# Kernel optimization log

Hardware: AMD Instinct MI355X
Metric: run time of the kernel (lower is better)

## Reference

```python
import jax, jax.numpy as jnp
import numpy as np

D = 300   # hidden dim (Linear(300,300))
L = 160   # seq len, forced by W3 = Linear(160,1)


def _linear(x, W, b):
    # torch Linear: x @ W.T + b, W is (out, in)
    return jnp.matmul(x, W.T) + b


def setup_inputs() -> dict:
    key = jax.random.key(0)
    ks = jax.random.split(key, 16)
    B = 1024
    s = 1.0 / np.sqrt(D)
    inp = {
        'T_feature': jax.random.normal(ks[0], (B, L, D), jnp.float32),
        'CD_feature': jax.random.normal(ks[1], (B, L, D), jnp.float32),
        'Wproj': jax.random.normal(ks[2], (D, D), jnp.float32) * s,
        'bproj': jnp.zeros((D,), jnp.float32),
        'WqT_w': jax.random.normal(ks[3], (D, D), jnp.float32) * s,
        'WqT_b': jnp.zeros((D,), jnp.float32),
        'WqCD_w': jax.random.normal(ks[4], (D, D), jnp.float32) * s,
        'WqCD_b': jnp.zeros((D,), jnp.float32),
        'WkT_w': jax.random.normal(ks[5], (D, D), jnp.float32) * s,
        'WkT_b': jnp.zeros((D,), jnp.float32),
        'WkCD_w': jax.random.normal(ks[6], (D, D), jnp.float32) * s,
        'WkCD_b': jnp.zeros((D,), jnp.float32),
        'W3_w': jax.random.normal(ks[7], (1, L), jnp.float32) * (1.0 / np.sqrt(L)),
        'W3_b': jnp.zeros((1,), jnp.float32),
    }
    return inp


def reference(T_feature, CD_feature, Wproj, bproj, WqT_w, WqT_b, WqCD_w, WqCD_b,
              WkT_w, WkT_b, WkCD_w, WkCD_b, W3_w, W3_b):
    sqrt_d = jnp.sqrt(jnp.float32(D))
    proj_T = _linear(T_feature, Wproj, bproj)     # (B, L, D)
    proj_CD = _linear(CD_feature, Wproj, bproj)   # (B, L, D)

    # N_tensor @ proj_T is just the mean over tokens (weights 1/Len)
    mean_T = jnp.mean(proj_T, axis=1, keepdims=True)          # (B, 1, D)
    qT = _linear(mean_T, WqT_w, WqT_b)                        # (B, 1, D)
    kT = _linear(proj_T, WkT_w, WkT_b)                        # (B, L, D)
    alphaT = jnp.einsum('bqd,bkd->bqk', qT, kT) / sqrt_d      # (B, 1, L)
    ZT = jax.nn.sigmoid(alphaT)

    qCD = _linear(proj_CD, WqCD_w, WqCD_b)                    # (B, L, D)
    kCD = _linear(proj_CD, WkCD_w, WkCD_b)                    # (B, L, D)
    alphaCD = jnp.einsum('bqd,bkd->bqk', qCD, kCD) / sqrt_d   # (B, L, L)
    ZCD = jax.nn.sigmoid(alphaCD)

    # The per-token loop+cat is a plain broadcast multiply: Mt[:,i,:] = ZCD[:,i,:] * ZT[:,0,:]
    Mt = ZCD * ZT                                             # (B, L, L)
    alpha_f = jax.nn.softmax(_linear(Mt, W3_w, W3_b), axis=1) # (B, L, 1)

    # Second loop is a per-token scalar scale: HCD[:,i,:] = alpha_f[:,i,0] * proj_CD[:,i,:]
    HCD = alpha_f * proj_CD                                   # (B, L, D)
    return (proj_T, HCD)
```

## Files before the change

kernel.cpp:

```cpp
#include <hip/hip_runtime.h>
#include <hip/hip_bf16.h>


typedef __attribute__((ext_vector_type(8))) short short8;
typedef __attribute__((ext_vector_type(4))) float f32x4;

#define DP 320

__device__ __forceinline__ unsigned short f2bf(float x) {
  unsigned int u = __builtin_bit_cast(unsigned int, x);
  u += 0x7FFFu + ((u >> 16) & 1u);
  return (unsigned short)(u >> 16);
}
__device__ __forceinline__ float bf2f(unsigned short h) {
  unsigned int u = ((unsigned int)h) << 16;
  return __builtin_bit_cast(float, u);
}
__device__ __forceinline__ void gload16(const void* g, void* l) {
  __builtin_amdgcn_global_load_lds(
      (const __attribute__((address_space(1))) unsigned int*)g,
      (__attribute__((address_space(3))) unsigned int*)l, 16, 0, 0);
}
__device__ __forceinline__ float sigm(float x) { return 1.0f / (1.0f + __expf(-x)); }
__device__ __forceinline__ int swz640(int row, int g) { return row * 640 + ((g ^ (row & 7)) << 4); }
__device__ __forceinline__ int swzY(int row, int g) { return row * 128 + ((g ^ (row & 7)) << 4); }

__global__ void wb_k(const float* __restrict__ W, unsigned short* __restrict__ Wb) {
  int n = blockIdx.x, k = threadIdx.x;
  unsigned short v = 0;
  if (n < 300 && k < 300) v = f2bf(W[n * 300 + k]);
  Wb[n * DP + k] = v;
}

__global__ void crossdot_k(const float* __restrict__ Wa, const float* __restrict__ ba,
                           const float* __restrict__ Wc, const float* __restrict__ bc,
                           unsigned short* __restrict__ out_h, float* __restrict__ out_f,
                           float scale) {
  int n = blockIdx.x, c = threadIdx.x;
  float v = 0.f;
  if (n <= 300 && c <= 300) {
    for (int o = 0; o < 300; ++o) {
      float a = (c < 300) ? Wa[o * 300 + c] : ba[o];
      float b = (n < 300) ? Wc[o * 300 + n] : bc[o];
      v += a * b;
    }
    v *= scale;
  }
  if (out_h) out_h[n * DP + c] = f2bf(v);
  else       out_f[n * DP + c] = v;
}

__global__ __launch_bounds__(512)
void gemm_k(const float* __restrict__ Tsrc, const float* __restrict__ CDsrc,
            const unsigned short* __restrict__ Wb, const float* __restrict__ bias,
            float* __restrict__ Of, unsigned short* __restrict__ Oh) {
  __shared__ __align__(16) unsigned short As[2][128 * 40];
  __shared__ __align__(16) unsigned short Bs[2][320 * 40];
  const int tid = threadIdx.x, wid = tid >> 6, lane = tid & 63;
  const int mode = blockIdx.y;
  const float* __restrict__ A = mode ? CDsrc : Tsrc;
  const long m0 = (long)blockIdx.x * 128;
  const int lr = lane & 15, lk = (lane >> 4) * 8;
  const int rm = (wid >> 2) * 64, cn = (wid & 3) * 80;

  f32x4 acc[4][5];
#pragma unroll
  for (int i = 0; i < 4; ++i)
#pragma unroll
    for (int j = 0; j < 5; ++j) acc[i][j] = (f32x4){0.f, 0.f, 0.f, 0.f};

  auto stageA = [&](int buf, int k0) {
    const int row = tid >> 2, cg = (tid & 3) * 8;
    const float* p = A + (m0 + row) * 300 + k0 + cg;
    short8 h;
    if (k0 + cg + 8 <= 300) {
      f32x4 x0 = *(const f32x4*)p, x1 = *(const f32x4*)(p + 4);
#pragma unroll
      for (int j = 0; j < 4; ++j) { h[j] = (short)f2bf(x0[j]); h[j + 4] = (short)f2bf(x1[j]); }
    } else {
#pragma unroll
      for (int j = 0; j < 8; ++j) {
        float v = (k0 + cg + j < 300) ? p[j] : 0.f;
        h[j] = (short)f2bf(v);
      }
    }
    *(short8*)&As[buf][row * 40 + cg] = h;
  };
  auto stageB = [&](int buf, int k0) {
#pragma unroll
    for (int it = 0; it < 3; ++it) {
      int idx = tid + it * 512;
      if (idx < 1280) {
        int row = idx >> 2, cg = (idx & 3) * 8;
        short8 h = *(const short8*)(Wb + row * DP + k0 + cg);
        *(short8*)&Bs[buf][row * 40 + cg] = h;
      }
    }
  };

  stageA(0, 0); stageB(0, 0);
  __syncthreads();
  int buf = 0;
  for (int kc = 0; kc < 10; ++kc) {
    if (kc < 9) { stageA(buf ^ 1, (kc + 1) * 32); stageB(buf ^ 1, (kc + 1) * 32); }
    short8 a[4], bb[5];
#pragma unroll
    for (int mf = 0; mf < 4; ++mf)
      a[mf] = *(const short8*)&As[buf][(rm + mf * 16 + lr) * 40 + lk];
#pragma unroll
    for (int nf = 0; nf < 5; ++nf)
      bb[nf] = *(const short8*)&Bs[buf][(cn + nf * 16 + lr) * 40 + lk];
#pragma unroll
    for (int mf = 0; mf < 4; ++mf)
#pragma unroll
      for (int nf = 0; nf < 5; ++nf)
        acc[mf][nf] = __builtin_amdgcn_mfma_f32_16x16x32_bf16(a[mf], bb[nf], acc[mf][nf], 0, 0, 0);
    __syncthreads();
    buf ^= 1;
  }

#pragma unroll
  for (int mf = 0; mf < 4; ++mf)
#pragma unroll
    for (int nf = 0; nf < 5; ++nf) {
      const int col = cn + nf * 16 + lr;
      const float bv = (col < 300) ? bias[col] : 0.f;
#pragma unroll
      for (int r = 0; r < 4; ++r) {
        const long row = m0 + rm + mf * 16 + (lane >> 4) * 4 + r;
        float v = acc[mf][nf][r] + bv;
        if (mode == 0) {
          if (col < 300) Of[row * 300 + col] = v;
        } else {
          unsigned short u = (col < 300) ? f2bf(v)
                            : ((col == 300) ? f2bf(1.0f) : (unsigned short)0);
          Oh[row * DP + col] = u;
        }
      }
    }
}

__global__ __launch_bounds__(320)
void gate_k(const float* __restrict__ projT, const float* __restrict__ Pmat,
            float* __restrict__ ZT) {
  __shared__ float mt[304];
  __shared__ float vv[304];
  const int b = blockIdx.x, tid = threadIdx.x, wid = tid >> 6, lane = tid & 63;
  const float* p = projT + (size_t)b * 48000;
  if (tid < 300) {
    float s = 0.f;
#pragma unroll 4
    for (int l = 0; l < 160; ++l) s += p[l * 300 + tid];
    mt[tid] = s * (1.0f / 160.0f);
  }
  __syncthreads();
  if (tid <= 300) {
    float s = Pmat[300 * DP + tid];
    for (int a = 0; a < 300; ++a) s += Pmat[a * DP + tid] * mt[a];
    vv[tid] = s;
  }
  __syncthreads();
  for (int j = wid * 32; j < wid * 32 + 32; ++j) {
    const float* row = p + j * 300;
    float s = 0.f;
    for (int c = lane; c < 300; c += 64) s += vv[c] * row[c];
#pragma unroll
    for (int m = 1; m < 64; m <<= 1) s += __shfl_xor(s, m, 64);
    if (lane == 0) ZT[b * 160 + j] = sigm(s + vv[300]);
  }
}

__global__ __launch_bounds__(640)
void finale_k(const unsigned short* __restrict__ P, const unsigned short* __restrict__ Maug,
              const float* __restrict__ ZT, const float* __restrict__ W3w,
              float* __restrict__ out) {
  __shared__ __align__(16) unsigned short Ps[160 * 320];
  __shared__ __align__(16) unsigned short Ms[32 * 320];
  __shared__ __align__(16) unsigned short Ys[160 * 64];
  __shared__ float t_arr[160];
  __shared__ float s_part[5][160];
  __shared__ float s_arr[160];
  __shared__ float red0;

  const int b = blockIdx.x, tid = threadIdx.x, wid = tid >> 6, lane = tid & 63;
  const int lr = lane & 15, hi = lane >> 4;
  const unsigned short* Pb = P + (size_t)b * 160 * DP;

  if (tid < 160) t_arr[tid] = ZT[b * 160 + tid] * W3w[tid];

#pragma unroll
  for (int it = 0; it < 10; ++it) {
    int o = it * 640 + tid;
    int row = o / 40, g = o - row * 40;
    gload16(Pb + row * DP + ((g ^ (row & 7)) << 3),
            (char*)Ps + ((it * 640 + (wid << 6)) << 4));
  }
  short8 mreg[2];
  int mrow[2], mg[2];
#pragma unroll
  for (int it = 0; it < 2; ++it) {
    int idx = tid + it * 640;
    mrow[it] = idx / 40; mg[it] = idx - mrow[it] * 40;
    mreg[it] = *(const short8*)(Maug + mrow[it] * DP + mg[it] * 8);
  }
  __syncthreads();
#pragma unroll
  for (int it = 0; it < 2; ++it)
    *(short8*)((char*)Ms + swz640(mrow[it], mg[it])) = mreg[it];
  short8 a_pre[10];
#pragma unroll
  for (int kk = 0; kk < 10; ++kk)
    a_pre[kk] = *(const short8*)((const char*)Ps + swz640(16 * wid + lr, kk * 4 + hi));
  __syncthreads();

  f32x4 acc_s[5][2];
#pragma unroll
  for (int i = 0; i < 5; ++i)
#pragma unroll
    for (int j = 0; j < 2; ++j) acc_s[i][j] = (f32x4){0.f, 0.f, 0.f, 0.f};
  const int wm = wid / 5, wn = wid - wm * 5;

  for (int nc = 0; nc < 10; ++nc) {
    if (nc < 9) {
#pragma unroll
      for (int it = 0; it < 2; ++it)
        mreg[it] = *(const short8*)(Maug + ((nc + 1) * 32 + mrow[it]) * DP + mg[it] * 8);
    }
    f32x4 accy0 = (f32x4){0.f, 0.f, 0.f, 0.f}, accy1 = accy0;
#pragma unroll
    for (int kk = 0; kk < 10; ++kk) {
      short8 b0 = *(const short8*)((const char*)Ms + swz640(lr, kk * 4 + hi));
      short8 b1 = *(const short8*)((const char*)Ms + swz640(16 + lr, kk * 4 + hi));
      accy0 = __builtin_amdgcn_mfma_f32_16x16x32_bf16(a_pre[kk], b0, accy0, 0, 0, 0);
      accy1 = __builtin_amdgcn_mfma_f32_16x16x32_bf16(a_pre[kk], b1, accy1, 0, 0, 0);
    }
    __syncthreads();
#pragma unroll
    for (int r = 0; r < 4; ++r) {
      int row = 16 * wid + hi * 4 + r;
      int c0 = lr, c1 = 16 + lr;
      *(unsigned short*)((char*)Ys + swzY(row, c0 >> 3) + ((c0 & 7) << 1)) = f2bf(accy0[r]);
      *(unsigned short*)((char*)Ys + swzY(row, c1 >> 3) + ((c1 & 7) << 1)) = f2bf(accy1[r]);
    }
    if (nc < 9) {
#pragma unroll
      for (int it = 0; it < 2; ++it)
        *(short8*)((char*)Ms + swz640(mrow[it], mg[it])) = mreg[it];
    }
    __syncthreads();
#pragma unroll
    for (int mf = 0; mf < 5; ++mf) {
      short8 a = *(const short8*)((const char*)Ys + swzY(80 * wm + mf * 16 + lr, hi));
#pragma unroll
      for (int nf = 0; nf < 2; ++nf) {
        short8 bv = *(const short8*)((const char*)Ps + swz640(32 * wn + nf * 16 + lr, nc * 4 + hi));
        acc_s[mf][nf] = __builtin_amdgcn_mfma_f32_16x16x32_bf16(a, bv, acc_s[mf][nf], 0, 0, 0);
      }
    }
    __syncthreads();
  }

  float tv0 = t_arr[32 * wn + lr], tv1 = t_arr[32 * wn + 16 + lr];
  float pp[5][4];
#pragma unroll
  for (int mf = 0; mf < 5; ++mf)
#pragma unroll
    for (int r = 0; r < 4; ++r)
      pp[mf][r] = sigm(acc_s[mf][0][r]) * tv0 + sigm(acc_s[mf][1][r]) * tv1;
#pragma unroll
  for (int m = 1; m < 16; m <<= 1)
#pragma unroll
    for (int mf = 0; mf < 5; ++mf)
#pragma unroll
      for (int r = 0; r < 4; ++r)
        pp[mf][r] += __shfl_xor(pp[mf][r], m, 64);
  if (lr == 0) {
#pragma unroll
    for (int mf = 0; mf < 5; ++mf)
#pragma unroll
      for (int r = 0; r < 4; ++r)
        s_part[wn][80 * wm + mf * 16 + hi * 4 + r] = pp[mf][r];
  }
  __syncthreads();
  if (tid < 160)
    s_arr[tid] = s_part[0][tid] + s_part[1][tid] + s_part[2][tid] + s_part[3][tid] + s_part[4][tid];
  __syncthreads();
  if (wid == 0) {
    float v0 = s_arr[lane], v1 = s_arr[lane + 64];
    float v2 = (lane < 32) ? s_arr[lane + 128] : -3.0e38f;
    float mx = fmaxf(fmaxf(v0, v1), v2);
#pragma unroll
    for (int m = 1; m < 64; m <<= 1) mx = fmaxf(mx, __shfl_xor(mx, m, 64));
    float e0 = __expf(v0 - mx), e1 = __expf(v1 - mx);
    float e2 = (lane < 32) ? __expf(v2 - mx) : 0.f;
    s_arr[lane] = e0; s_arr[lane + 64] = e1;
    if (lane < 32) s_arr[lane + 128] = e2;
    float sm = e0 + e1 + e2;
#pragma unroll
    for (int m = 1; m < 64; m <<= 1) sm += __shfl_xor(sm, m, 64);
    if (lane == 0) red0 = 1.0f / sm;
  }
  __syncthreads();
  const float inv = red0;
  float* ob = out + (size_t)b * 48000;
  for (int e = tid; e < 48000; e += 640) {
    int i = e / 300, c = e - i * 300;
    unsigned short pv = *(const unsigned short*)((const char*)Ps + swz640(i, c >> 3) + ((c & 7) << 1));
    ob[e] = s_arr[i] * inv * bf2f(pv);
  }
}

extern "C" void kernel_launch(void* const* d_in, const int* in_sizes, int n_in,
                              void* d_out, int out_size, void* d_ws, size_t ws_size,
                              hipStream_t stream) {
  (void)in_sizes; (void)n_in; (void)out_size; (void)ws_size;
  const float* T      = (const float*)d_in[0];
  const float* CD     = (const float*)d_in[1];
  const float* Wproj  = (const float*)d_in[2];
  const float* bproj  = (const float*)d_in[3];
  const float* WqT_w  = (const float*)d_in[4];
  const float* WqT_b  = (const float*)d_in[5];
  const float* WqCD_w = (const float*)d_in[6];
  const float* WqCD_b = (const float*)d_in[7];
  const float* WkT_w  = (const float*)d_in[8];
  const float* WkT_b  = (const float*)d_in[9];
  const float* WkCD_w = (const float*)d_in[10];
  const float* WkCD_b = (const float*)d_in[11];
  const float* W3_w   = (const float*)d_in[12];

  char* ws = (char*)d_ws;
  size_t off = 0;
  auto alloc = [&](size_t bytes) { void* p = ws + off; off = (off + bytes + 255) & ~(size_t)255; return p; };
  unsigned short* pCD   = (unsigned short*)alloc((size_t)1024 * 160 * DP * 2);
  unsigned short* Wb    = (unsigned short*)alloc((size_t)DP * DP * 2);
  unsigned short* MaugT = (unsigned short*)alloc((size_t)DP * DP * 2);
  float* Pmat = (float*)alloc((size_t)DP * DP * 4);
  float* ZT   = (float*)alloc((size_t)1024 * 160 * 4);

  float* projT = (float*)d_out;
  float* HCD   = (float*)d_out + (size_t)49152000;

  const float isd = 1.0f / sqrtf(300.0f);

  wb_k<<<dim3(320), dim3(320), 0, stream>>>(Wproj, Wb);
  crossdot_k<<<dim3(320), dim3(320), 0, stream>>>(WqCD_w, WqCD_b, WkCD_w, WkCD_b, MaugT, nullptr, isd);
  crossdot_k<<<dim3(320), dim3(320), 0, stream>>>(WkT_w, WkT_b, WqT_w, WqT_b, nullptr, Pmat, isd);

  gemm_k<<<dim3(1280, 2), dim3(512), 0, stream>>>(T, CD, Wb, bproj, projT, pCD);
  gate_k<<<dim3(1024), dim3(320), 0, stream>>>(projT, Pmat, ZT);
  finale_k<<<dim3(1024), dim3(640), 0, stream>>>(pCD, MaugT, ZT, W3_w, HCD);
}
```

Baseline: 627.4 us.

## Pre-convert inputs to bf16, enlarge GEMM tiles, hoist Y=P·M GEMM out of finale

Adds a separate kernel that converts T and CD to swizzled bf16 in workspace. The projection GEMM becomes a 256x320 tile with 64-wide K chunks loaded by async global-to-LDS copies. The per-batch Y = pCD·Maug product moves out of the finale kernel into a third pass of the same GEMM kernel written to global memory, so finale only computes Y·P^T, the softmax and the scaled output with vectorised reads. The aim is more MFMA reuse and less per-block conversion and LDS staging, in exchange for extra global round trips for the bf16 copies and Y, plus an added conversion pass.

```diff
diff --git a/kernel.cpp b/kernel.cpp
--- a/kernel.cpp
+++ b/kernel.cpp
@@ -22,14 +22,14 @@
       (__attribute__((address_space(3))) unsigned int*)l, 16, 0, 0);
 }
 __device__ __forceinline__ float sigm(float x) { return 1.0f / (1.0f + __expf(-x)); }
-__device__ __forceinline__ int swz640(int row, int g) { return row * 640 + ((g ^ (row & 7)) << 4); }
-__device__ __forceinline__ int swzY(int row, int g) { return row * 128 + ((g ^ (row & 7)) << 4); }
+__device__ __forceinline__ int swzc(int r, int c) {
+  return (c & ~63) | ((((c >> 3) & 7) ^ (r & 7)) << 3) | (c & 7);
+}
 
 __global__ void wb_k(const float* __restrict__ W, unsigned short* __restrict__ Wb) {
-  int n = blockIdx.x, k = threadIdx.x;
-  unsigned short v = 0;
-  if (n < 300 && k < 300) v = f2bf(W[n * 300 + k]);
-  Wb[n * DP + k] = v;
+  int n = blockIdx.x, c = threadIdx.x;
+  unsigned short v = (n < 300 && c < 300) ? f2bf(W[n * 300 + c]) : (unsigned short)0;
+  Wb[n * DP + swzc(n, c)] = v;
 }
 
 __global__ void crossdot_k(const float* __restrict__ Wa, const float* __restrict__ ba,
@@ -46,75 +46,102 @@
     }
     v *= scale;
   }
-  if (out_h) out_h[n * DP + c] = f2bf(v);
+  if (out_h) out_h[n * DP + swzc(n, c)] = f2bf(v);
   else       out_f[n * DP + c] = v;
 }
 
+__global__ __launch_bounds__(256)
+void cvt_k(const float* __restrict__ T, const float* __restrict__ CD,
+           unsigned short* __restrict__ Abf) {
+  unsigned idx = blockIdx.x * 256 + threadIdx.x;
+  if (idx >= 327680u * 40u) return;
+  unsigned row = idx / 40u, G = idx - row * 40u;
+  int kc = G >> 3, sg = G & 7;
+  int col0 = kc * 64 + (sg ^ ((int)row & 7)) * 8;
+  const float* base = (row < 163840u) ? T + (size_t)row * 300
+                                      : CD + (size_t)(row - 163840u) * 300;
+  short8 h;
+  if (col0 + 8 <= 300) {
+    f32x4 x0 = *(const f32x4*)(base + col0), x1 = *(const f32x4*)(base + col0 + 4);
+#pragma unroll
+    for (int j = 0; j < 4; ++j) { h[j] = (short)f2bf(x0[j]); h[j + 4] = (short)f2bf(x1[j]); }
+  } else {
+#pragma unroll
+    for (int j = 0; j < 8; ++j) {
+      int c = col0 + j;
+      h[j] = (short)((c < 300) ? f2bf(base[c]) : (unsigned short)0);
+    }
+  }
+  *(short8*)(Abf + (size_t)row * DP + G * 8) = h;
+}
+
 __global__ __launch_bounds__(512)
-void gemm_k(const float* __restrict__ Tsrc, const float* __restrict__ CDsrc,
-            const unsigned short* __restrict__ Wb, const float* __restrict__ bias,
-            float* __restrict__ Of, unsigned short* __restrict__ Oh) {
-  __shared__ __align__(16) unsigned short As[2][128 * 40];
-  __shared__ __align__(16) unsigned short Bs[2][320 * 40];
+void gemm_k(const unsigned short* __restrict__ Abf, const unsigned short* __restrict__ pCDg,
+            const unsigned short* __restrict__ Wb, const unsigned short* __restrict__ Maug,
+            const float* __restrict__ bias, float* __restrict__ Of,
+            unsigned short* __restrict__ pCDout, unsigned short* __restrict__ Yout,
+            int mode_base) {
+  __shared__ __align__(16) unsigned short As[2][256 * 64];
+  __shared__ __align__(16) unsigned short Bs[2][320 * 64];
   const int tid = threadIdx.x, wid = tid >> 6, lane = tid & 63;
-  const int mode = blockIdx.y;
-  const float* __restrict__ A = mode ? CDsrc : Tsrc;
-  const long m0 = (long)blockIdx.x * 128;
-  const int lr = lane & 15, lk = (lane >> 4) * 8;
-  const int rm = (wid >> 2) * 64, cn = (wid & 3) * 80;
-
-  f32x4 acc[4][5];
+  const int lr = lane & 15, hi = lane >> 4;
+  const int mode = mode_base + blockIdx.y;
+  const unsigned short* __restrict__ A =
+      (mode == 0) ? Abf : (mode == 1) ? Abf + (size_t)163840 * DP : pCDg;
+  const unsigned short* __restrict__ Bm = (mode == 2) ? Maug : Wb;
+  const size_t m0 = (size_t)blockIdx.x * 256;
+
+  f32x4 acc[4][10];
 #pragma unroll
   for (int i = 0; i < 4; ++i)
 #pragma unroll
-    for (int j = 0; j < 5; ++j) acc[i][j] = (f32x4){0.f, 0.f, 0.f, 0.f};
-
-  auto stageA = [&](int buf, int k0) {
-    const int row = tid >> 2, cg = (tid & 3) * 8;
-    const float* p = A + (m0 + row) * 300 + k0 + cg;
-    short8 h;
-    if (k0 + cg + 8 <= 300) {
-      f32x4 x0 = *(const f32x4*)p, x1 = *(const f32x4*)(p + 4);
-#pragma unroll
-      for (int j = 0; j < 4; ++j) { h[j] = (short)f2bf(x0[j]); h[j + 4] = (short)f2bf(x1[j]); }
-    } else {
-#pragma unroll
-      for (int j = 0; j < 8; ++j) {
-        float v = (k0 + cg + j < 300) ? p[j] : 0.f;
-        h[j] = (short)f2bf(v);
+    for (int j = 0; j < 10; ++j) acc[i][j] = (f32x4){0.f, 0.f, 0.f, 0.f};
+
+  auto stageA = [&](int buf, int kc) {
+#pragma unroll
+    for (int it = 0; it < 4; ++it) {
+      int idx = it * 512 + tid;
+      int row = idx >> 3, g = idx & 7;
+      gload16(A + (m0 + row) * DP + kc * 64 + g * 8, (char*)As[buf] + idx * 16);
+    }
+  };
+  auto stageB = [&](int buf, int kc) {
+#pragma unroll
+    for (int it = 0; it < 5; ++it) {
+      int idx = it * 512 + tid;
+      int row = idx >> 3, g = idx & 7;
+      gload16(Bm + (size_t)row * DP + kc * 64 + g * 8, (char*)Bs[buf] + idx * 16);
+    }
+  };
+
+  stageA(0, 0); stageB(0, 0);
+  __syncthreads();
+  int buf = 0;
+  const int rm = (wid >> 1) * 64, cn = (wid & 1) * 160;
+  for (int kc = 0; kc < 5; ++kc) {
+    if (kc < 4) { stageA(buf ^ 1, kc + 1); stageB(buf ^ 1, kc + 1); }
+#pragma unroll
+    for (int kk = 0; kk < 2; ++kk) {
+      const int slot = ((kk * 4 + hi) ^ lr) & 7;
+      short8 a[4];
+#pragma unroll
+      for (int mf = 0; mf < 4; ++mf)
+        a[mf] = *(const short8*)((const char*)As[buf] + (rm + mf * 16 + lr) * 128 + slot * 16);
+#pragma unroll
+      for (int nh = 0; nh < 2; ++nh) {
+        short8 b[5];
+#pragma unroll
+        for (int nf = 0; nf < 5; ++nf)
+          b[nf] = *(const short8*)((const char*)Bs[buf] +
+                                   (cn + (nh * 5 + nf) * 16 + lr) * 128 + slot * 16);
+#pragma unroll
+        for (int mf = 0; mf < 4; ++mf)
+#pragma unroll
+          for (int nf = 0; nf < 5; ++nf)
+            acc[mf][nh * 5 + nf] =
+                __builtin_amdgcn_mfma_f32_16x16x32_bf16(a[mf], b[nf], acc[mf][nh * 5 + nf], 0, 0, 0);
       }
     }
-    *(short8*)&As[buf][row * 40 + cg] = h;
-  };
-  auto stageB = [&](int buf, int k0) {
-#pragma unroll
-    for (int it = 0; it < 3; ++it) {
-      int idx = tid + it * 512;
-      if (idx < 1280) {
-        int row = idx >> 2, cg = (idx & 3) * 8;
-        short8 h = *(const short8*)(Wb + row * DP + k0 + cg);
-        *(short8*)&Bs[buf][row * 40 + cg] = h;
-      }
-    }
-  };
-
-  stageA(0, 0); stageB(0, 0);
-  __syncthreads();
-  int buf = 0;
-  for (int kc = 0; kc < 10; ++kc) {
-    if (kc < 9) { stageA(buf ^ 1, (kc + 1) * 32); stageB(buf ^ 1, (kc + 1) * 32); }
-    short8 a[4], bb[5];
-#pragma unroll
-    for (int mf = 0; mf < 4; ++mf)
-      a[mf] = *(const short8*)&As[buf][(rm + mf * 16 + lr) * 40 + lk];
-#pragma unroll
-    for (int nf = 0; nf < 5; ++nf)
-      bb[nf] = *(const short8*)&Bs[buf][(cn + nf * 16 + lr) * 40 + lk];
-#pragma unroll
-    for (int mf = 0; mf < 4; ++mf)
-#pragma unroll
-      for (int nf = 0; nf < 5; ++nf)
-        acc[mf][nf] = __builtin_amdgcn_mfma_f32_16x16x32_bf16(a[mf], bb[nf], acc[mf][nf], 0, 0, 0);
     __syncthreads();
     buf ^= 1;
   }
@@ -122,19 +149,21 @@
 #pragma unroll
   for (int mf = 0; mf < 4; ++mf)
 #pragma unroll
-    for (int nf = 0; nf < 5; ++nf) {
+    for (int nf = 0; nf < 10; ++nf) {
       const int col = cn + nf * 16 + lr;
-      const float bv = (col < 300) ? bias[col] : 0.f;
+      const float bv = (mode < 2 && col < 300) ? bias[col] : 0.f;
 #pragma unroll
       for (int r = 0; r < 4; ++r) {
-        const long row = m0 + rm + mf * 16 + (lane >> 4) * 4 + r;
+        const size_t row = m0 + rm + mf * 16 + hi * 4 + r;
         float v = acc[mf][nf][r] + bv;
         if (mode == 0) {
           if (col < 300) Of[row * 300 + col] = v;
         } else {
-          unsigned short u = (col < 300) ? f2bf(v)
-                            : ((col == 300) ? f2bf(1.0f) : (unsigned short)0);
-          Oh[row * DP + col] = u;
+          unsigned short u = (mode == 2) ? f2bf(v)
+                           : (col < 300) ? f2bf(v)
+                           : (col == 300) ? f2bf(1.0f) : (unsigned short)0;
+          unsigned short* dst = (mode == 1) ? pCDout : Yout;
+          dst[row * DP + swzc((int)row, col)] = u;
         }
       }
     }
@@ -170,120 +199,91 @@
   }
 }
 
-__global__ __launch_bounds__(640)
-void finale_k(const unsigned short* __restrict__ P, const unsigned short* __restrict__ Maug,
+__global__ __launch_bounds__(320)
+void finale_k(const unsigned short* __restrict__ Yg, const unsigned short* __restrict__ Pg,
               const float* __restrict__ ZT, const float* __restrict__ W3w,
               float* __restrict__ out) {
-  __shared__ __align__(16) unsigned short Ps[160 * 320];
-  __shared__ __align__(16) unsigned short Ms[32 * 320];
-  __shared__ __align__(16) unsigned short Ys[160 * 64];
+  __shared__ __align__(16) unsigned short Ps[160 * DP];
+  __shared__ __align__(16) unsigned short Ys[2][160 * 64];
   __shared__ float t_arr[160];
-  __shared__ float s_part[5][160];
   __shared__ float s_arr[160];
   __shared__ float red0;
-
   const int b = blockIdx.x, tid = threadIdx.x, wid = tid >> 6, lane = tid & 63;
   const int lr = lane & 15, hi = lane >> 4;
-  const unsigned short* Pb = P + (size_t)b * 160 * DP;
+  const unsigned short* Pb = Pg + (size_t)b * 160 * DP;
+  const unsigned short* Yb = Yg + (size_t)b * 160 * DP;
 
   if (tid < 160) t_arr[tid] = ZT[b * 160 + tid] * W3w[tid];
 
 #pragma unroll
-  for (int it = 0; it < 10; ++it) {
-    int o = it * 640 + tid;
-    int row = o / 40, g = o - row * 40;
-    gload16(Pb + row * DP + ((g ^ (row & 7)) << 3),
-            (char*)Ps + ((it * 640 + (wid << 6)) << 4));
-  }
-  short8 mreg[2];
-  int mrow[2], mg[2];
-#pragma unroll
-  for (int it = 0; it < 2; ++it) {
-    int idx = tid + it * 640;
-    mrow[it] = idx / 40; mg[it] = idx - mrow[it] * 40;
-    mreg[it] = *(const short8*)(Maug + mrow[it] * DP + mg[it] * 8);
-  }
-  __syncthreads();
-#pragma unroll
-  for (int it = 0; it < 2; ++it)
-    *(short8*)((char*)Ms + swz640(mrow[it], mg[it])) = mreg[it];
-  short8 a_pre[10];
-#pragma unroll
-  for (int kk = 0; kk < 10; ++kk)
-    a_pre[kk] = *(const short8*)((const char*)Ps + swz640(16 * wid + lr, kk * 4 + hi));
-  __syncthreads();
-
-  f32x4 acc_s[5][2];
-#pragma unroll
-  for (int i = 0; i < 5; ++i)
-#pragma unroll
-    for (int j = 0; j < 2; ++j) acc_s[i][j] = (f32x4){0.f, 0.f, 0.f, 0.f};
-  const int wm = wid / 5, wn = wid - wm * 5;
-
-  for (int nc = 0; nc < 10; ++nc) {
-    if (nc < 9) {
-#pragma unroll
-      for (int it = 0; it < 2; ++it)
-        mreg[it] = *(const short8*)(Maug + ((nc + 1) * 32 + mrow[it]) * DP + mg[it] * 8);
-    }
-    f32x4 accy0 = (f32x4){0.f, 0.f, 0.f, 0.f}, accy1 = accy0;
-#pragma unroll
-    for (int kk = 0; kk < 10; ++kk) {
-      short8 b0 = *(const short8*)((const char*)Ms + swz640(lr, kk * 4 + hi));
-      short8 b1 = *(const short8*)((const char*)Ms + swz640(16 + lr, kk * 4 + hi));
-      accy0 = __builtin_amdgcn_mfma_f32_16x16x32_bf16(a_pre[kk], b0, accy0, 0, 0, 0);
-      accy1 = __builtin_amdgcn_mfma_f32_16x16x32_bf16(a_pre[kk], b1, accy1, 0, 0, 0);
+  for (int it = 0; it < 20; ++it) {
+    int idx = it * 320 + tid;
+    gload16(Pb + (size_t)idx * 8, (char*)Ps + idx * 16);
+  }
+  auto stageY = [&](int buf, int kc) {
+#pragma unroll
+    for (int it = 0; it < 4; ++it) {
+      int idx = it * 320 + tid;
+      int row = idx >> 3, g = idx & 7;
+      gload16(Yb + (size_t)row * DP + kc * 64 + g * 8, (char*)Ys[buf] + idx * 16);
+    }
+  };
+
+  f32x4 acc[2][10];
+#pragma unroll
+  for (int i = 0; i < 2; ++i)
+#pragma unroll
+    for (int j = 0; j < 10; ++j) acc[i][j] = (f32x4){0.f, 0.f, 0.f, 0.f};
+
+  stageY(0, 0);
+  __syncthreads();
+  int buf = 0;
+  const int rm = wid * 32;
+  for (int kc = 0; kc < 5; ++kc) {
+    if (kc < 4) stageY(buf ^ 1, kc + 1);
+#pragma unroll
+    for (int kk = 0; kk < 2; ++kk) {
+      const int slot = ((kk * 4 + hi) ^ lr) & 7;
+      short8 a[2], bb[10];
+#pragma unroll
+      for (int mf = 0; mf < 2; ++mf)
+        a[mf] = *(const short8*)((const char*)Ys[buf] + (rm + mf * 16 + lr) * 128 + slot * 16);
+#pragma unroll
+      for (int nf = 0; nf < 10; ++nf)
+        bb[nf] = *(const short8*)((const char*)Ps + (nf * 16 + lr) * 640 + (kc * 8 + slot) * 16);
+#pragma unroll
+      for (int mf = 0; mf < 2; ++mf)
+#pragma unroll
+        for (int nf = 0; nf < 10; ++nf)
+          acc[mf][nf] = __builtin_amdgcn_mfma_f32_16x16x32_bf16(a[mf], bb[nf], acc[mf][nf], 0, 0, 0);
     }
     __syncthreads();
+    buf ^= 1;
+  }
+
+  float pp[2][4];
+#pragma unroll
+  for (int mf = 0; mf < 2; ++mf)
 #pragma unroll
     for (int r = 0; r < 4; ++r) {
-      int row = 16 * wid + hi * 4 + r;
-      int c0 = lr, c1 = 16 + lr;
-      *(unsigned short*)((char*)Ys + swzY(row, c0 >> 3) + ((c0 & 7) << 1)) = f2bf(accy0[r]);
-      *(unsigned short*)((char*)Ys + swzY(row, c1 >> 3) + ((c1 & 7) << 1)) = f2bf(accy1[r]);
-    }
-    if (nc < 9) {
-#pragma unroll
-      for (int it = 0; it < 2; ++it)
-        *(short8*)((char*)Ms + swz640(mrow[it], mg[it])) = mreg[it];
-    }
-    __syncthreads();
-#pragma unroll
-    for (int mf = 0; mf < 5; ++mf) {
-      short8 a = *(const short8*)((const char*)Ys + swzY(80 * wm + mf * 16 + lr, hi));
-#pragma unroll
-      for (int nf = 0; nf < 2; ++nf) {
-        short8 bv = *(const short8*)((const char*)Ps + swz640(32 * wn + nf * 16 + lr, nc * 4 + hi));
-        acc_s[mf][nf] = __builtin_amdgcn_mfma_f32_16x16x32_bf16(a, bv, acc_s[mf][nf], 0, 0, 0);
-      }
-    }
-    __syncthreads();
-  }
-
-  float tv0 = t_arr[32 * wn + lr], tv1 = t_arr[32 * wn + 16 + lr];
-  float pp[5][4];
-#pragma unroll
-  for (int mf = 0; mf < 5; ++mf)
-#pragma unroll
-    for (int r = 0; r < 4; ++r)
-      pp[mf][r] = sigm(acc_s[mf][0][r]) * tv0 + sigm(acc_s[mf][1][r]) * tv1;
+      float s = 0.f;
+#pragma unroll
+      for (int nf = 0; nf < 10; ++nf) s += sigm(acc[mf][nf][r]) * t_arr[nf * 16 + lr];
+      pp[mf][r] = s;
+    }
 #pragma unroll
   for (int m = 1; m < 16; m <<= 1)
 #pragma unroll
-    for (int mf = 0; mf < 5; ++mf)
+    for (int mf = 0; mf < 2; ++mf)
+#pragma unroll
+      for (int r = 0; r < 4; ++r) pp[mf][r] += __shfl_xor(pp[mf][r], m, 64);
+  if (lr == 0) {
+#pragma unroll
+    for (int mf = 0; mf < 2; ++mf)
 #pragma unroll
       for (int r = 0; r < 4; ++r)
-        pp[mf][r] += __shfl_xor(pp[mf][r], m, 64);
-  if (lr == 0) {
-#pragma unroll
-    for (int mf = 0; mf < 5; ++mf)
-#pragma unroll
-      for (int r = 0; r < 4; ++r)
-        s_part[wn][80 * wm + mf * 16 + hi * 4 + r] = pp[mf][r];
-  }
-  __syncthreads();
-  if (tid < 160)
-    s_arr[tid] = s_part[0][tid] + s_part[1][tid] + s_part[2][tid] + s_part[3][tid] + s_part[4][tid];
+        s_arr[rm + mf * 16 + hi * 4 + r] = pp[mf][r];
+  }
   __syncthreads();
   if (wid == 0) {
     float v0 = s_arr[lane], v1 = s_arr[lane + 64];
@@ -303,10 +303,21 @@
   __syncthreads();
   const float inv = red0;
   float* ob = out + (size_t)b * 48000;
-  for (int e = tid; e < 48000; e += 640) {
-    int i = e / 300, c = e - i * 300;
-    unsigned short pv = *(const unsigned short*)((const char*)Ps + swz640(i, c >> 3) + ((c & 7) << 1));
-    ob[e] = s_arr[i] * inv * bf2f(pv);
+#pragma unroll 2
+  for (int it = 0; it < 19; ++it) {
+    int idx = it * 320 + tid;
+    if (idx < 6080) {
+      int i = idx / 38, cg = idx - i * 38;
+      int sg = (cg & ~7) | ((cg & 7) ^ (i & 7));
+      short8 pv = *(const short8*)((const char*)Ps + i * 640 + sg * 16);
+      float sc = s_arr[i] * inv;
+      int c0 = cg * 8;
+#pragma unroll
+      for (int j = 0; j < 8; ++j) {
+        int c = c0 + j;
+        if (c < 300) ob[(size_t)i * 300 + c] = sc * bf2f((unsigned short)pv[j]);
+      }
+    }
   }
 }
 
@@ -331,7 +342,7 @@
   char* ws = (char*)d_ws;
   size_t off = 0;
   auto alloc = [&](size_t bytes) { void* p = ws + off; off = (off + bytes + 255) & ~(size_t)255; return p; };
-  unsigned short* pCD   = (unsigned short*)alloc((size_t)1024 * 160 * DP * 2);
+  unsigned short* Abf   = (unsigned short*)alloc((size_t)327680 * DP * 2);
   unsigned short* Wb    = (unsigned short*)alloc((size_t)DP * DP * 2);
   unsigned short* MaugT = (unsigned short*)alloc((size_t)DP * DP * 2);
   float* Pmat = (float*)alloc((size_t)DP * DP * 4);
@@ -339,14 +350,20 @@
 
   float* projT = (float*)d_out;
   float* HCD   = (float*)d_out + (size_t)49152000;
+  unsigned short* pCDg = Abf + (size_t)163840 * DP;
+  unsigned short* Yg   = Abf;
 
   const float isd = 1.0f / sqrtf(300.0f);
 
   wb_k<<<dim3(320), dim3(320), 0, stream>>>(Wproj, Wb);
   crossdot_k<<<dim3(320), dim3(320), 0, stream>>>(WqCD_w, WqCD_b, WkCD_w, WkCD_b, MaugT, nullptr, isd);
   crossdot_k<<<dim3(320), dim3(320), 0, stream>>>(WkT_w, WkT_b, WqT_w, WqT_b, nullptr, Pmat, isd);
-
-  gemm_k<<<dim3(1280, 2), dim3(512), 0, stream>>>(T, CD, Wb, bproj, projT, pCD);
+  cvt_k<<<dim3(51200), dim3(256), 0, stream>>>(T, CD, Abf);
+
+  gemm_k<<<dim3(640, 2), dim3(512), 0, stream>>>(Abf, pCDg, Wb, MaugT, bproj,
+                                                 projT, pCDg, Yg, 0);
   gate_k<<<dim3(1024), dim3(320), 0, stream>>>(projT, Pmat, ZT);
-  finale_k<<<dim3(1024), dim3(640), 0, stream>>>(pCD, MaugT, ZT, W3_w, HCD);
-}
+  gemm_k<<<dim3(640, 1), dim3(512), 0, stream>>>(Abf, pCDg, Wb, MaugT, bproj,
+                                                 projT, pCDg, Yg, 2);
+  finale_k<<<dim3(1024), dim3(320), 0, stream>>>(Yg, pCDg, ZT, W3_w, HCD);
+}
```

Measured after the change: 775.5 us. 23.6% more time.
